# Optimization experiments

Measured on AMD Instinct MI355X. Metric: run time of the kernel, lower is better.

Reference implementation:

```python
import jax, jax.numpy as jnp
import numpy as np

DIM = 2048
NUM_HEADS = 16
HEAD_DIM = DIM // NUM_HEADS
SCALE = 1.0 / float(np.sqrt(HEAD_DIM))


def setup_inputs() -> dict:
    key = jax.random.key(0)
    ks = jax.random.split(key, 7)
    B, L = 2, 2048
    x = jax.random.normal(ks[0], (B, L, DIM), dtype=jnp.float32)
    s = 1.0 / np.sqrt(DIM)
    # nn.Linear stores weight as [out, in]; y = x @ W.T + b
    Wq = jax.random.uniform(ks[1], (DIM, DIM), jnp.float32, -s, s)
    bq = jax.random.uniform(ks[2], (DIM,), jnp.float32, -s, s)
    Wk = jax.random.uniform(ks[3], (DIM, DIM), jnp.float32, -s, s)
    bk = jax.random.uniform(ks[4], (DIM,), jnp.float32, -s, s)
    Wv = jax.random.uniform(ks[5], (DIM, DIM), jnp.float32, -s, s)
    bv = jax.random.uniform(ks[6], (DIM,), jnp.float32, -s, s)
    return {"x": x, "Wq": Wq, "bq": bq, "Wk": Wk, "bk": bk, "Wv": Wv, "bv": bv}


def _attn(x, Wq, bq, Wk, bk, Wv, bv):
    B, L, D = x.shape
    H, Hd = NUM_HEADS, HEAD_DIM
    # projections: x @ W.T + b, then split heads -> [B, H, L, Hd]
    q = (x @ Wq.T + bq).reshape(B, L, H, Hd).transpose(0, 2, 1, 3)
    k = (x @ Wk.T + bk).reshape(B, L, H, Hd).transpose(0, 2, 1, 3)
    v = (x @ Wv.T + bv).reshape(B, L, H, Hd).transpose(0, 2, 1, 3)
    scores = jnp.einsum("bhqd,bhkd->bhqk", q, k) * SCALE  # [B,H,L,L]
    attn = jax.nn.softmax(scores, axis=-1)
    out = jnp.einsum("bhqk,bhkd->bhqd", attn, v)
    return out.transpose(0, 2, 1, 3).reshape(B, L, D)


def reference(x, Wq, bq, Wk, bk, Wv, bv):
    return _attn(x, Wq, bq, Wk, bk, Wv, bv)
```

## Files before the change

kernel.cpp:

```cpp
#include <hip/hip_runtime.h>
#include <stdint.h>

typedef unsigned short u16;
typedef __attribute__((ext_vector_type(8))) short short8;
typedef __attribute__((ext_vector_type(4))) float f32x4;
typedef __attribute__((ext_vector_type(16))) float f32x16;

#define ATTN_SCALE 0.08838834764831845f

__device__ __forceinline__ u16 f2bf(float f) {
  union { float f; uint32_t u; } a; a.f = f;
  return (u16)((a.u + 0x7fffu + ((a.u >> 16) & 1u)) >> 16);
}

__device__ __forceinline__ void async16(const u16* g, u16* lds) {
  __builtin_amdgcn_global_load_lds(
      (const __attribute__((address_space(1))) void*)g,
      (__attribute__((address_space(3))) void*)lds, 16, 0, 0);
}

__global__ void cvt_kernel(const float* __restrict__ src, u16* __restrict__ dst, int n8) {
  int i = blockIdx.x * 256 + threadIdx.x;
  if (i >= n8) return;
  const float4* s4 = (const float4*)src;
  float4 a = s4[2 * i], c = s4[2 * i + 1];
  union { u16 h[8]; uint4 v; } o;
  o.h[0] = f2bf(a.x); o.h[1] = f2bf(a.y); o.h[2] = f2bf(a.z); o.h[3] = f2bf(a.w);
  o.h[4] = f2bf(c.x); o.h[5] = f2bf(c.y); o.h[6] = f2bf(c.z); o.h[7] = f2bf(c.w);
  ((uint4*)dst)[i] = o.v;
}

__global__ void cvtw_kernel(const float* __restrict__ w0, const float* __restrict__ w1,
                            const float* __restrict__ w2, u16* __restrict__ dst) {
  int z = blockIdx.y;
  const float* src = (z == 0) ? w0 : (z == 1) ? w1 : w2;
  int i = blockIdx.x * 256 + threadIdx.x;
  const float4* s4 = (const float4*)src;
  float4 a = s4[2 * i], c = s4[2 * i + 1];
  union { u16 h[8]; uint4 v; } o;
  o.h[0] = f2bf(a.x); o.h[1] = f2bf(a.y); o.h[2] = f2bf(a.z); o.h[3] = f2bf(a.w);
  o.h[4] = f2bf(c.x); o.h[5] = f2bf(c.y); o.h[6] = f2bf(c.z); o.h[7] = f2bf(c.w);
  ((uint4*)(dst + (size_t)z * 4194304))[i] = o.v;
}

__global__ __launch_bounds__(256, 2) void qkv_gemm(
    const u16* __restrict__ xb, const u16* __restrict__ Wb,
    const float* __restrict__ bq, const float* __restrict__ bk, const float* __restrict__ bv,
    u16* __restrict__ qkv) {
  __shared__ __align__(16) u16 As[128 * 32];
  __shared__ __align__(16) u16 Bs[128 * 32];
  const int z = blockIdx.z;
  const int n0 = blockIdx.x * 128, m0 = blockIdx.y * 128;
  const u16* Bw = Wb + (size_t)z * (2048u * 2048u);
  const float* bias = (z == 0) ? bq : (z == 1) ? bk : bv;
  u16* dst = qkv + (size_t)z * 8388608u;
  const int t = threadIdx.x, wave = t >> 6, lane = t & 63;
  const int wm = wave >> 1, wn = wave & 1, l15 = lane & 15, quad = lane >> 4;
  const int lr = lane >> 2, lc = (lane & 3) * 8;

  f32x4 acc[4][4];
  const f32x4 vzero = {0.f, 0.f, 0.f, 0.f};
#pragma unroll
  for (int i = 0; i < 4; ++i)
#pragma unroll
    for (int j = 0; j < 4; ++j) acc[i][j] = vzero;

  for (int k0 = 0; k0 < 2048; k0 += 32) {
    __syncthreads();
    async16(xb + (size_t)(m0 + wave * 16 + lr) * 2048 + k0 + lc,       &As[wave * 512]);
    async16(xb + (size_t)(m0 + (wave + 4) * 16 + lr) * 2048 + k0 + lc, &As[(wave + 4) * 512]);
    async16(Bw + (size_t)(n0 + wave * 16 + lr) * 2048 + k0 + lc,       &Bs[wave * 512]);
    async16(Bw + (size_t)(n0 + (wave + 4) * 16 + lr) * 2048 + k0 + lc, &Bs[(wave + 4) * 512]);
    __syncthreads();

    short8 af[4], bfr[4];
#pragma unroll
    for (int i = 0; i < 4; ++i)
      af[i] = *(const short8*)&As[(wm * 64 + i * 16 + l15) * 32 + quad * 8];
#pragma unroll
    for (int j = 0; j < 4; ++j)
      bfr[j] = *(const short8*)&Bs[(wn * 64 + j * 16 + l15) * 32 + quad * 8];
#pragma unroll
    for (int i = 0; i < 4; ++i)
#pragma unroll
      for (int j = 0; j < 4; ++j)
        acc[i][j] = __builtin_amdgcn_mfma_f32_16x16x32_bf16(af[i], bfr[j], acc[i][j], 0, 0, 0);
  }

#pragma unroll
  for (int j = 0; j < 4; ++j) {
    const int col = n0 + wn * 64 + j * 16 + l15;
    const float bb_ = bias[col];
    const int h = col >> 7, hd = col & 127;
#pragma unroll
    for (int i = 0; i < 4; ++i) {
#pragma unroll
      for (int r = 0; r < 4; ++r) {
        const int row = m0 + wm * 64 + i * 16 + quad * 4 + r;
        const int bb = row >> 11, l = row & 2047;
        const u16 v = f2bf(acc[i][j][r] + bb_);
        if (z == 2)
          dst[((size_t)(bb * 16 + h) * 128 + hd) * 2048 + l] = v;
        else
          dst[((size_t)(bb * 16 + h) * 2048 + l) * 128 + hd] = v;
      }
    }
  }
}

__global__ __launch_bounds__(256, 2) void attn_kernel(
    const u16* __restrict__ Qg,
    const u16* __restrict__ Kg,
    const u16* __restrict__ Vtg,
    float* __restrict__ out) {
  __shared__ __align__(16) u16 Ks[128 * 128];
  __shared__ __align__(16) u16 Vs[128 * 128];
  const int bh = blockIdx.y, q0 = blockIdx.x * 128;
  const int t = threadIdx.x, wave = t >> 6, lane = t & 63;
  const int l31 = lane & 31, h = lane >> 5, r15 = lane & 15;
  const u16* Qp = Qg + (size_t)bh * 262144;
  const u16* Kp = Kg + (size_t)bh * 262144;
  const u16* Vp = Vtg + (size_t)bh * 262144;
  const int b = bh >> 4, hd = bh & 15;
  const int qrow = q0 + wave * 32 + l31;

  short8 qf[8];
#pragma unroll
  for (int s = 0; s < 8; ++s)
    qf[s] = *(const short8*)&Qp[(size_t)qrow * 128 + s * 16 + h * 8];

  f32x16 oac[4];
#pragma unroll
  for (int dt = 0; dt < 4; ++dt)
#pragma unroll
    for (int r = 0; r < 16; ++r) oac[dt][r] = 0.f;
  float den = 0.f;

  for (int kt = 0; kt < 16; ++kt) {
    const int k0 = kt * 128;
    __syncthreads();
#pragma unroll
    for (int p = 0; p < 8; ++p) {
      const int cid = (wave * 8 + p) * 64 + lane;
      const int row = cid >> 4;
      const int g = r15 ^ (row & 15);
      async16(Kp + (size_t)(k0 + row) * 128 + g * 8, &Ks[(wave * 8 + p) * 512]);
      async16(Vp + (size_t)row * 2048 + k0 + g * 8,  &Vs[(wave * 8 + p) * 512]);
    }
    __syncthreads();

#pragma unroll
    for (int T = 0; T < 4; ++T) {
      f32x16 sc;
#pragma unroll
      for (int r = 0; r < 16; ++r) sc[r] = 0.f;
#pragma unroll
      for (int s = 0; s < 8; ++s) {
        const short8 kf = *(const short8*)&Ks[(T * 32 + l31) * 128 + (((2 * s + h) ^ r15) * 8)];
        sc = __builtin_amdgcn_mfma_f32_32x32x16_bf16(kf, qf[s], sc, 0, 0, 0);
      }
      uint32_t pp[8];
#pragma unroll
      for (int i = 0; i < 8; ++i) {
        float e0 = __expf(fminf(fmaxf(sc[2 * i] * ATTN_SCALE, -80.f), 80.f));
        float e1 = __expf(fminf(fmaxf(sc[2 * i + 1] * ATTN_SCALE, -80.f), 80.f));
        den += e0 + e1;
        pp[i] = ((uint32_t)f2bf(e1) << 16) | (uint32_t)f2bf(e0);
      }
      uint32_t x[8];
#pragma unroll
      for (int i = 0; i < 8; ++i) x[i] = __shfl_xor(pp[i], 32, 64);
#pragma unroll
      for (int ks = 0; ks < 2; ++ks) {
        const int o0 = ks * 4;
        union { uint32_t u[4]; short8 s8; } bf;
        bf.u[0] = h ? x[o0 + 2] : pp[o0 + 0];
        bf.u[1] = h ? x[o0 + 3] : pp[o0 + 1];
        bf.u[2] = h ? pp[o0 + 2] : x[o0 + 0];
        bf.u[3] = h ? pp[o0 + 3] : x[o0 + 1];
        const int gk = T * 4 + ks * 2 + h;
#pragma unroll
        for (int dt = 0; dt < 4; ++dt) {
          const short8 vf = *(const short8*)&Vs[(dt * 32 + l31) * 128 + ((gk ^ r15) * 8)];
          oac[dt] = __builtin_amdgcn_mfma_f32_32x32x16_bf16(vf, bf.s8, oac[dt], 0, 0, 0);
        }
      }
    }
  }

  den += __shfl_xor(den, 32, 64);
  const float inv = 1.f / den;

#pragma unroll
  for (int dt = 0; dt < 4; ++dt) {
#pragma unroll
    for (int g4 = 0; g4 < 4; ++g4) {
      float4 o;
      o.x = oac[dt][4 * g4 + 0] * inv;
      o.y = oac[dt][4 * g4 + 1] * inv;
      o.z = oac[dt][4 * g4 + 2] * inv;
      o.w = oac[dt][4 * g4 + 3] * inv;
      const int d = dt * 32 + g4 * 8 + h * 4;
      *(float4*)&out[((size_t)(b * 2048 + qrow)) * 2048 + hd * 128 + d] = o;
    }
  }
}

extern "C" void kernel_launch(void* const* d_in, const int* in_sizes, int n_in,
                              void* d_out, int out_size, void* d_ws, size_t ws_size,
                              hipStream_t stream) {
  const float* x  = (const float*)d_in[0];
  const float* Wq = (const float*)d_in[1];
  const float* bq = (const float*)d_in[2];
  const float* Wk = (const float*)d_in[3];
  const float* bk = (const float*)d_in[4];
  const float* Wv = (const float*)d_in[5];
  const float* bv = (const float*)d_in[6];
  float* out = (float*)d_out;
  if (ws_size < 92274688u) return;

  u16* xb  = (u16*)d_ws;
  u16* Wb  = xb + 8388608;
  u16* qkv = Wb + 12582912;

  cvt_kernel<<<4096, 256, 0, stream>>>(x, xb, 1048576);
  cvtw_kernel<<<dim3(2048, 3), 256, 0, stream>>>(Wq, Wk, Wv, Wb);
  qkv_gemm<<<dim3(16, 32, 3), 256, 0, stream>>>(xb, Wb, bq, bk, bv, qkv);
  attn_kernel<<<dim3(16, 32), 256, 0, stream>>>(qkv, qkv + 8388608, qkv + 16777216, out);
}
```

Measured before the change: 353.9 us.

## Double-buffer LDS in GEMM and attention, switch GEMM to 32x32 MFMA

The QKV GEMM now double-buffers its LDS tiles, issuing the next K-slice's async loads before computing on the current one. It also moves from 16x16x32 to 32x32x16 MFMAs, vectorizes the V-transposed stores, and raises the launch-bounds occupancy hint to 3. The attention kernel likewise double-buffers 64-key K/V tiles with adjusted XOR swizzles, so each step needs one barrier instead of two and loads overlap with compute. It also simplifies exp clamping and the bf16 packing (round-half-up instead of round-to-nearest-even). The goal is to hide global-to-LDS latency behind MFMA work. The cost is more LDS per block and slight rounding differences.

```diff
diff --git a/kernel.cpp b/kernel.cpp
--- a/kernel.cpp
+++ b/kernel.cpp
@@ -3,7 +3,6 @@
 
 typedef unsigned short u16;
 typedef __attribute__((ext_vector_type(8))) short short8;
-typedef __attribute__((ext_vector_type(4))) float f32x4;
 typedef __attribute__((ext_vector_type(16))) float f32x16;
 
 #define ATTN_SCALE 0.08838834764831845f
@@ -43,66 +42,89 @@
   ((uint4*)(dst + (size_t)z * 4194304))[i] = o.v;
 }
 
-__global__ __launch_bounds__(256, 2) void qkv_gemm(
+__global__ __launch_bounds__(256, 3) void qkv_gemm(
     const u16* __restrict__ xb, const u16* __restrict__ Wb,
     const float* __restrict__ bq, const float* __restrict__ bk, const float* __restrict__ bv,
     u16* __restrict__ qkv) {
-  __shared__ __align__(16) u16 As[128 * 32];
-  __shared__ __align__(16) u16 Bs[128 * 32];
+  __shared__ __align__(16) u16 As[2][128 * 32];
+  __shared__ __align__(16) u16 Bs[2][128 * 32];
   const int z = blockIdx.z;
   const int n0 = blockIdx.x * 128, m0 = blockIdx.y * 128;
   const u16* Bw = Wb + (size_t)z * (2048u * 2048u);
   const float* bias = (z == 0) ? bq : (z == 1) ? bk : bv;
   u16* dst = qkv + (size_t)z * 8388608u;
   const int t = threadIdx.x, wave = t >> 6, lane = t & 63;
-  const int wm = wave >> 1, wn = wave & 1, l15 = lane & 15, quad = lane >> 4;
-  const int lr = lane >> 2, lc = (lane & 3) * 8;
-
-  f32x4 acc[4][4];
-  const f32x4 vzero = {0.f, 0.f, 0.f, 0.f};
-#pragma unroll
-  for (int i = 0; i < 4; ++i)
-#pragma unroll
-    for (int j = 0; j < 4; ++j) acc[i][j] = vzero;
-
-  for (int k0 = 0; k0 < 2048; k0 += 32) {
+  const int wm = wave >> 1, wn = wave & 1, l31 = lane & 31, h = lane >> 5;
+
+  const int cid0 = wave * 128 + lane;
+  f32x16 acc[2][2];
+#pragma unroll
+  for (int i = 0; i < 2; ++i)
+#pragma unroll
+    for (int j = 0; j < 2; ++j)
+#pragma unroll
+      for (int r = 0; r < 16; ++r) acc[i][j][r] = 0.f;
+
+#pragma unroll 1
+  for (int n = 0; n < 64; ++n) {
+    if (n == 0) {
+#pragma unroll
+      for (int p = 0; p < 2; ++p) {
+        const int cid = cid0 + p * 64, row = cid >> 2, col = (cid & 3) * 8;
+        async16(xb + (size_t)(m0 + row) * 2048 + col, &As[0][cid * 8]);
+        async16(Bw + (size_t)(n0 + row) * 2048 + col, &Bs[0][cid * 8]);
+      }
+    }
     __syncthreads();
-    async16(xb + (size_t)(m0 + wave * 16 + lr) * 2048 + k0 + lc,       &As[wave * 512]);
-    async16(xb + (size_t)(m0 + (wave + 4) * 16 + lr) * 2048 + k0 + lc, &As[(wave + 4) * 512]);
-    async16(Bw + (size_t)(n0 + wave * 16 + lr) * 2048 + k0 + lc,       &Bs[wave * 512]);
-    async16(Bw + (size_t)(n0 + (wave + 4) * 16 + lr) * 2048 + k0 + lc, &Bs[(wave + 4) * 512]);
-    __syncthreads();
-
-    short8 af[4], bfr[4];
-#pragma unroll
-    for (int i = 0; i < 4; ++i)
-      af[i] = *(const short8*)&As[(wm * 64 + i * 16 + l15) * 32 + quad * 8];
-#pragma unroll
-    for (int j = 0; j < 4; ++j)
-      bfr[j] = *(const short8*)&Bs[(wn * 64 + j * 16 + l15) * 32 + quad * 8];
-#pragma unroll
-    for (int i = 0; i < 4; ++i)
-#pragma unroll
-      for (int j = 0; j < 4; ++j)
-        acc[i][j] = __builtin_amdgcn_mfma_f32_16x16x32_bf16(af[i], bfr[j], acc[i][j], 0, 0, 0);
-  }
-
-#pragma unroll
-  for (int j = 0; j < 4; ++j) {
-    const int col = n0 + wn * 64 + j * 16 + l15;
+    const int cur = n & 1;
+    if (n + 1 < 64) {
+      const int k1 = (n + 1) * 32;
+#pragma unroll
+      for (int p = 0; p < 2; ++p) {
+        const int cid = cid0 + p * 64, row = cid >> 2, col = (cid & 3) * 8;
+        async16(xb + (size_t)(m0 + row) * 2048 + k1 + col, &As[cur ^ 1][cid * 8]);
+        async16(Bw + (size_t)(n0 + row) * 2048 + k1 + col, &Bs[cur ^ 1][cid * 8]);
+      }
+    }
+#pragma unroll
+    for (int ks = 0; ks < 2; ++ks) {
+      short8 af[2], bf[2];
+#pragma unroll
+      for (int i = 0; i < 2; ++i)
+        af[i] = *(const short8*)&As[cur][(wm * 64 + i * 32 + l31) * 32 + ks * 16 + h * 8];
+#pragma unroll
+      for (int j = 0; j < 2; ++j)
+        bf[j] = *(const short8*)&Bs[cur][(wn * 64 + j * 32 + l31) * 32 + ks * 16 + h * 8];
+#pragma unroll
+      for (int i = 0; i < 2; ++i)
+#pragma unroll
+        for (int j = 0; j < 2; ++j)
+          acc[i][j] = __builtin_amdgcn_mfma_f32_32x32x16_bf16(af[i], bf[j], acc[i][j], 0, 0, 0);
+    }
+  }
+
+#pragma unroll
+  for (int j = 0; j < 2; ++j) {
+    const int col = n0 + wn * 64 + j * 32 + l31;
     const float bb_ = bias[col];
-    const int h = col >> 7, hd = col & 127;
-#pragma unroll
-    for (int i = 0; i < 4; ++i) {
-#pragma unroll
-      for (int r = 0; r < 4; ++r) {
-        const int row = m0 + wm * 64 + i * 16 + quad * 4 + r;
-        const int bb = row >> 11, l = row & 2047;
-        const u16 v = f2bf(acc[i][j][r] + bb_);
-        if (z == 2)
-          dst[((size_t)(bb * 16 + h) * 128 + hd) * 2048 + l] = v;
-        else
-          dst[((size_t)(bb * 16 + h) * 2048 + l) * 128 + hd] = v;
+    const int hh = col >> 7, hd = col & 127;
+#pragma unroll
+    for (int i = 0; i < 2; ++i) {
+#pragma unroll
+      for (int g = 0; g < 4; ++g) {
+        const int lbase = m0 + wm * 64 + i * 32 + 8 * g + 4 * h;
+        const int bb = lbase >> 11, l0 = lbase & 2047;
+        if (z == 2) {
+          union { u16 q[4]; ushort2 d[2]; } pk;
+#pragma unroll
+          for (int rr = 0; rr < 4; ++rr) pk.q[rr] = f2bf(acc[i][j][4 * g + rr] + bb_);
+          *(uint2*)&dst[((size_t)(bb * 16 + hh) * 128 + hd) * 2048 + l0] = *(uint2*)pk.q;
+        } else {
+#pragma unroll
+          for (int rr = 0; rr < 4; ++rr)
+            dst[((size_t)(bb * 16 + hh) * 2048 + (l0 + rr)) * 128 + hd] =
+                f2bf(acc[i][j][4 * g + rr] + bb_);
+        }
       }
     }
   }
@@ -113,11 +135,11 @@
     const u16* __restrict__ Kg,
     const u16* __restrict__ Vtg,
     float* __restrict__ out) {
-  __shared__ __align__(16) u16 Ks[128 * 128];
-  __shared__ __align__(16) u16 Vs[128 * 128];
+  __shared__ __align__(16) u16 Ks[2][64 * 128];
+  __shared__ __align__(16) u16 Vs[2][128 * 64];
   const int bh = blockIdx.y, q0 = blockIdx.x * 128;
   const int t = threadIdx.x, wave = t >> 6, lane = t & 63;
-  const int l31 = lane & 31, h = lane >> 5, r15 = lane & 15;
+  const int l31 = lane & 31, h = lane >> 5;
   const u16* Qp = Qg + (size_t)bh * 262144;
   const u16* Kp = Kg + (size_t)bh * 262144;
   const u16* Vp = Vtg + (size_t)bh * 262144;
@@ -135,37 +157,53 @@
 #pragma unroll
     for (int r = 0; r < 16; ++r) oac[dt][r] = 0.f;
   float den = 0.f;
-
-  for (int kt = 0; kt < 16; ++kt) {
-    const int k0 = kt * 128;
+  const int cidK = wave * 256 + lane;
+
+#pragma unroll 1
+  for (int n = 0; n < 32; ++n) {
+    if (n == 0) {
+#pragma unroll
+      for (int p = 0; p < 4; ++p) {
+        const int cid = cidK + p * 64;
+        const int rk = cid >> 4, gk = (cid & 15) ^ (rk & 15);
+        async16(Kp + (size_t)rk * 128 + gk * 8, &Ks[0][cid * 8]);
+        const int rv = cid >> 3, gv = (cid & 7) ^ (rv & 7);
+        async16(Vp + (size_t)rv * 2048 + gv * 8, &Vs[0][cid * 8]);
+      }
+    }
     __syncthreads();
-#pragma unroll
-    for (int p = 0; p < 8; ++p) {
-      const int cid = (wave * 8 + p) * 64 + lane;
-      const int row = cid >> 4;
-      const int g = r15 ^ (row & 15);
-      async16(Kp + (size_t)(k0 + row) * 128 + g * 8, &Ks[(wave * 8 + p) * 512]);
-      async16(Vp + (size_t)row * 2048 + k0 + g * 8,  &Vs[(wave * 8 + p) * 512]);
-    }
-    __syncthreads();
-
-#pragma unroll
-    for (int T = 0; T < 4; ++T) {
+    const int cur = n & 1;
+    if (n + 1 < 32) {
+      const int k1 = (n + 1) * 64;
+#pragma unroll
+      for (int p = 0; p < 4; ++p) {
+        const int cid = cidK + p * 64;
+        const int rk = cid >> 4, gk = (cid & 15) ^ (rk & 15);
+        async16(Kp + (size_t)(k1 + rk) * 128 + gk * 8, &Ks[cur ^ 1][cid * 8]);
+        const int rv = cid >> 3, gv = (cid & 7) ^ (rv & 7);
+        async16(Vp + (size_t)rv * 2048 + k1 + gv * 8, &Vs[cur ^ 1][cid * 8]);
+      }
+    }
+
+#pragma unroll
+    for (int T = 0; T < 2; ++T) {
+      const int krow = T * 32 + l31;
       f32x16 sc;
 #pragma unroll
       for (int r = 0; r < 16; ++r) sc[r] = 0.f;
 #pragma unroll
       for (int s = 0; s < 8; ++s) {
-        const short8 kf = *(const short8*)&Ks[(T * 32 + l31) * 128 + (((2 * s + h) ^ r15) * 8)];
+        const short8 kf = *(const short8*)&Ks[cur][(krow * 16 + (((2 * s + h) ^ (krow & 15)))) * 8];
         sc = __builtin_amdgcn_mfma_f32_32x32x16_bf16(kf, qf[s], sc, 0, 0, 0);
       }
       uint32_t pp[8];
 #pragma unroll
       for (int i = 0; i < 8; ++i) {
-        float e0 = __expf(fminf(fmaxf(sc[2 * i] * ATTN_SCALE, -80.f), 80.f));
-        float e1 = __expf(fminf(fmaxf(sc[2 * i + 1] * ATTN_SCALE, -80.f), 80.f));
+        const float e0 = __expf(fminf(sc[2 * i] * ATTN_SCALE, 80.f));
+        const float e1 = __expf(fminf(sc[2 * i + 1] * ATTN_SCALE, 80.f));
         den += e0 + e1;
-        pp[i] = ((uint32_t)f2bf(e1) << 16) | (uint32_t)f2bf(e0);
+        union { float f; uint32_t u; } u0, u1; u0.f = e0; u1.f = e1;
+        pp[i] = ((u1.u + 0x8000u) & 0xffff0000u) | ((u0.u + 0x8000u) >> 16);
       }
       uint32_t x[8];
 #pragma unroll
@@ -173,16 +211,17 @@
 #pragma unroll
       for (int ks = 0; ks < 2; ++ks) {
         const int o0 = ks * 4;
-        union { uint32_t u[4]; short8 s8; } bf;
-        bf.u[0] = h ? x[o0 + 2] : pp[o0 + 0];
-        bf.u[1] = h ? x[o0 + 3] : pp[o0 + 1];
-        bf.u[2] = h ? pp[o0 + 2] : x[o0 + 0];
-        bf.u[3] = h ? pp[o0 + 3] : x[o0 + 1];
+        union { uint32_t u[4]; short8 s8; } bfp;
+        bfp.u[0] = h ? x[o0 + 2] : pp[o0 + 0];
+        bfp.u[1] = h ? x[o0 + 3] : pp[o0 + 1];
+        bfp.u[2] = h ? pp[o0 + 2] : x[o0 + 0];
+        bfp.u[3] = h ? pp[o0 + 3] : x[o0 + 1];
         const int gk = T * 4 + ks * 2 + h;
 #pragma unroll
         for (int dt = 0; dt < 4; ++dt) {
-          const short8 vf = *(const short8*)&Vs[(dt * 32 + l31) * 128 + ((gk ^ r15) * 8)];
-          oac[dt] = __builtin_amdgcn_mfma_f32_32x32x16_bf16(vf, bf.s8, oac[dt], 0, 0, 0);
+          const int vrow = dt * 32 + l31;
+          const short8 vf = *(const short8*)&Vs[cur][(vrow * 8 + (gk ^ (vrow & 7))) * 8];
+          oac[dt] = __builtin_amdgcn_mfma_f32_32x32x16_bf16(vf, bfp.s8, oac[dt], 0, 0, 0);
         }
       }
     }
@@ -190,7 +229,6 @@
 
   den += __shfl_xor(den, 32, 64);
   const float inv = 1.f / den;
-
 #pragma unroll
   for (int dt = 0; dt < 4; ++dt) {
 #pragma unroll
```

Result: slower. 366.0 us (+3.4%).
